# Kernel optimization log

Hardware: AMD Instinct MI355X
Metric: run time of the kernel (lower is better)

Reference implementation:

```python
import jax, jax.numpy as jnp
import numpy as np

B, T, D_IN, H = 1024, 512, 32, 64


def setup_inputs() -> dict:
    key = jax.random.key(0)
    ks = jax.random.split(key, 16)
    s_in = 1.0 / np.sqrt(H)  # torch LSTM init scale 1/sqrt(hidden)
    inp = {
        "x": jax.random.normal(ks[0], (B, T, D_IN), dtype=jnp.float32),
        # layer 0
        "Wih0": jax.random.uniform(ks[1], (4 * H, D_IN), minval=-s_in, maxval=s_in),
        "Whh0": jax.random.uniform(ks[2], (4 * H, H), minval=-s_in, maxval=s_in),
        "bih0": jax.random.uniform(ks[3], (4 * H,), minval=-s_in, maxval=s_in),
        "bhh0": jax.random.uniform(ks[4], (4 * H,), minval=-s_in, maxval=s_in),
        # layer 1
        "Wih1": jax.random.uniform(ks[5], (4 * H, H), minval=-s_in, maxval=s_in),
        "Whh1": jax.random.uniform(ks[6], (4 * H, H), minval=-s_in, maxval=s_in),
        "bih1": jax.random.uniform(ks[7], (4 * H,), minval=-s_in, maxval=s_in),
        "bhh1": jax.random.uniform(ks[8], (4 * H,), minval=-s_in, maxval=s_in),
        # head: Linear(H, H//2) -> ReLU -> Linear(H//2, 1)
        "W1": jax.random.uniform(ks[9], (H // 2, H), minval=-s_in, maxval=s_in),
        "b1": jax.random.uniform(ks[10], (H // 2,), minval=-s_in, maxval=s_in),
        "W2": jax.random.uniform(ks[11], (1, H // 2), minval=-1.0 / np.sqrt(H // 2), maxval=1.0 / np.sqrt(H // 2)),
        "b2": jax.random.uniform(ks[12], (1,), minval=-1.0 / np.sqrt(H // 2), maxval=1.0 / np.sqrt(H // 2)),
    }
    return inp


def _lstm_layer(x, Wih, Whh, bih, bhh):
    # x: [B, T, D]; returns all hidden states [B, T, H]
    b = x.shape[0]
    xT = jnp.swapaxes(x, 0, 1)  # [T, B, D]
    h0 = jnp.zeros((b, H), dtype=x.dtype)
    c0 = jnp.zeros((b, H), dtype=x.dtype)
    bias = bih + bhh

    def step(carry, xt):
        h, c = carry
        z = xt @ Wih.T + h @ Whh.T + bias  # [B, 4H]
        i, f, g, o = jnp.split(z, 4, axis=-1)  # torch gate order: i, f, g, o
        i = jax.nn.sigmoid(i)
        f = jax.nn.sigmoid(f)
        g = jnp.tanh(g)
        o = jax.nn.sigmoid(o)
        c = f * c + i * g
        h = o * jnp.tanh(c)
        return (h, c), h

    _, hs = jax.lax.scan(step, (h0, c0), xT)
    return jnp.swapaxes(hs, 0, 1)  # [B, T, H]


def reference(x, Wih0, Whh0, bih0, bhh0, Wih1, Whh1, bih1, bhh1, W1, b1, W2, b2):
    h1 = _lstm_layer(x, Wih0, Whh0, bih0, bhh0)   # [B, T, H]
    h2 = _lstm_layer(h1, Wih1, Whh1, bih1, bhh1)  # [B, T, H] (dropout = identity, eval)
    last = h2[:, -1]                              # [B, H]
    hidden = jax.nn.relu(last @ W1.T + b1)        # [B, H//2]
    out = hidden @ W2.T + b2                      # [B, 1]
    return out[:, 0]                              # [B]
```

## Files before the change

kernel.cpp:

```cpp
#include <hip/hip_runtime.h>

#define T       512
#define DIN     32
#define HCELLS  64
#define NB      16
#define TB      512
#define GRID    64

typedef _Float16 half8  __attribute__((ext_vector_type(8)));
typedef _Float16 half4v __attribute__((ext_vector_type(4)));
typedef _Float16 half2v __attribute__((ext_vector_type(2)));
typedef float    float4v __attribute__((ext_vector_type(4)));

#define STRX    40
#define STRH    72
#define XH_OFF  0
#define H0H_OFF (2*16*STRX)
#define H1H_OFF (H0H_OFF + 2*16*STRH)
#define SB_HALFS (H1H_OFF + 2*16*STRH)

#define LOG2E   1.44269504f
#define SLOG2E  2.88539008f

__device__ __forceinline__ int xidx(int p, int n, int k) { return (p * 16 + n) * STRX + k; }
__device__ __forceinline__ int hidx(int p, int n, int k) { return (p * 16 + n) * STRH + k; }

__device__ __forceinline__ void cvt8(const float* v, half8& hi) {
    #pragma unroll
    for (int e = 0; e < 8; ++e) hi[e] = (_Float16)v[e];
}

__device__ __forceinline__ void cell_update(const float4v acc[4], float* cs,
                                            half4v& hh, float* hout)
{
    #pragma unroll
    for (int r = 0; r < 4; ++r) {
        float ei = __builtin_amdgcn_exp2f(acc[0][r]);
        float ef = __builtin_amdgcn_exp2f(acc[1][r]);
        float G2 = __builtin_amdgcn_exp2f(acc[2][r]);
        float I  = 1.0f + ei, F = 1.0f + ef;
        float Gp = 1.0f + G2;
        float Gms = fmaf(SLOG2E, G2, -SLOG2E);
        float P   = I * Gp;
        float num = fmaf(F, Gms, cs[r] * P);
        float csn = num * __builtin_amdgcn_rcpf(F * P);
        csn = fminf(fmaxf(csn, -50.0f), 50.0f);
        cs[r] = csn;
        float eo = __builtin_amdgcn_exp2f(acc[3][r]);
        float C2 = __builtin_amdgcn_exp2f(csn);
        float O  = 1.0f + eo;
        float Cp = 1.0f + C2, Cm = C2 - 1.0f;
        float h  = Cm * __builtin_amdgcn_rcpf(O * Cp);
        if (hout) hout[r] = h;
        hh[r] = (_Float16)h;
    }
}

__global__ void __launch_bounds__(TB, 2)
lstm2_mfma_kernel(const float* __restrict__ x,
                  const float* __restrict__ Wih0, const float* __restrict__ Whh0,
                  const float* __restrict__ bih0, const float* __restrict__ bhh0,
                  const float* __restrict__ Wih1, const float* __restrict__ Whh1,
                  const float* __restrict__ bih1, const float* __restrict__ bhh1,
                  const float* __restrict__ W1,   const float* __restrict__ b1,
                  const float* __restrict__ W2,   const float* __restrict__ b2,
                  float* __restrict__ out)
{
    const int tid  = threadIdx.x;
    const int wid  = tid >> 6;
    const int grp  = wid >> 2;
    const int wl   = wid & 3;
    const int lane = tid & 63;
    const int n16  = lane & 15;
    const int q    = lane >> 4;
    const int j0   = wl * 16 + q * 4;
    const int b0   = blockIdx.x * NB;

    __shared__ __align__(16) _Float16 SB[SB_HALFS];
    __shared__ __align__(16) float HS[16 * 68 + 16 * 33];

    const float gsc[4] = {-LOG2E, -LOG2E, SLOG2E, -LOG2E};

    half8 ah[4][4];
    float4v biasv[4];

    #pragma unroll
    for (int l = 0; l < 4; ++l) {
        const int row = (l * 4 + wl) * 16 + n16;
        const float g = gsc[l];
        float v[8];
        if (grp == 0) {
            {
                const float4* p = (const float4*)(Wih0 + row * DIN + q * 8);
                float4 u0 = p[0], u1 = p[1];
                v[0]=g*u0.x; v[1]=g*u0.y; v[2]=g*u0.z; v[3]=g*u0.w;
                v[4]=g*u1.x; v[5]=g*u1.y; v[6]=g*u1.z; v[7]=g*u1.w;
                cvt8(v, ah[l][0]);
            }
            #pragma unroll
            for (int kt = 1; kt < 3; ++kt) {
                const float4* p = (const float4*)(Whh0 + row * HCELLS + (kt - 1) * 32 + q * 8);
                float4 u0 = p[0], u1 = p[1];
                v[0]=g*u0.x; v[1]=g*u0.y; v[2]=g*u0.z; v[3]=g*u0.w;
                v[4]=g*u1.x; v[5]=g*u1.y; v[6]=g*u1.z; v[7]=g*u1.w;
                cvt8(v, ah[l][kt]);
            }
            const int r0 = l * 64 + j0;
            float4v bi = *(const float4v*)(bih0 + r0);
            float4v bh = *(const float4v*)(bhh0 + r0);
            biasv[l] = (bi + bh) * g;
        } else {
            #pragma unroll
            for (int kt = 0; kt < 4; ++kt) {
                const float* base = (kt < 2) ? (Wih1 + row * HCELLS + kt * 32)
                                             : (Whh1 + row * HCELLS + (kt - 2) * 32);
                const float4* p = (const float4*)(base + q * 8);
                float4 u0 = p[0], u1 = p[1];
                v[0]=g*u0.x; v[1]=g*u0.y; v[2]=g*u0.z; v[3]=g*u0.w;
                v[4]=g*u1.x; v[5]=g*u1.y; v[6]=g*u1.z; v[7]=g*u1.w;
                cvt8(v, ah[l][kt]);
            }
            const int r0 = l * 64 + j0;
            float4v bi = *(const float4v*)(bih1 + r0);
            float4v bh = *(const float4v*)(bhh1 + r0);
            biasv[l] = (bi + bh) * g;
        }
    }

    for (int i = tid; i < SB_HALFS / 2; i += TB) ((int*)SB)[i] = 0;

    const int nx = tid >> 4;
    const int kp = (tid & 15) * 2;
    const float* xp0 = (grp == 0) ? (x + (size_t)(b0 + nx) * T * DIN + kp) : nullptr;
    __syncthreads();
    if (grp == 0) {
        float2 xv = *(const float2*)xp0;
        half2v hi = {(_Float16)xv.x, (_Float16)xv.y};
        *(half2v*)&SB[XH_OFF + xidx(0, nx, kp)] = hi;
    }
    __syncthreads();

    float cs[4] = {0, 0, 0, 0};
    float hlast[4];
    const float* xp = (grp == 0) ? (xp0 + DIN) : nullptr;

    #pragma unroll 2
    for (int t = 0; t < T; ++t) {
        const int pr = t & 1, pw = pr ^ 1;

        if (grp == 0) {
            float2 xv;
            const bool havex = (t + 1 < T);
            if (havex) xv = *(const float2*)xp;
            xp += DIN;

            float4v acc[4];
            #pragma unroll
            for (int l = 0; l < 4; ++l) acc[l] = biasv[l];
            {
                half8 bh = *(const half8*)&SB[XH_OFF + xidx(pr, n16, q * 8)];
                #pragma unroll
                for (int l = 0; l < 4; ++l)
                    acc[l] = __builtin_amdgcn_mfma_f32_16x16x32_f16(ah[l][0], bh, acc[l], 0, 0, 0);
            }
            #pragma unroll
            for (int kt = 1; kt < 3; ++kt) {
                half8 bh = *(const half8*)&SB[H0H_OFF + hidx(pr, n16, (kt - 1) * 32 + q * 8)];
                #pragma unroll
                for (int l = 0; l < 4; ++l)
                    acc[l] = __builtin_amdgcn_mfma_f32_16x16x32_f16(ah[l][kt], bh, acc[l], 0, 0, 0);
            }
            half4v hh;
            cell_update(acc, cs, hh, nullptr);
            *(half4v*)&SB[H0H_OFF + hidx(pw, n16, j0)] = hh;
            if (havex) {
                half2v hi = {(_Float16)xv.x, (_Float16)xv.y};
                *(half2v*)&SB[XH_OFF + xidx(pw, nx, kp)] = hi;
            }
        } else if (t > 0) {
            float4v acc[4];
            #pragma unroll
            for (int l = 0; l < 4; ++l) acc[l] = biasv[l];
            #pragma unroll
            for (int kt = 0; kt < 4; ++kt) {
                half8 bh = (kt < 2)
                    ? *(const half8*)&SB[H0H_OFF + hidx(pr, n16, kt * 32 + q * 8)]
                    : *(const half8*)&SB[H1H_OFF + hidx(pw, n16, (kt - 2) * 32 + q * 8)];
                #pragma unroll
                for (int l = 0; l < 4; ++l)
                    acc[l] = __builtin_amdgcn_mfma_f32_16x16x32_f16(ah[l][kt], bh, acc[l], 0, 0, 0);
            }
            half4v hh;
            cell_update(acc, cs, hh, nullptr);
            *(half4v*)&SB[H1H_OFF + hidx(pr, n16, j0)] = hh;
        }
        __syncthreads();
    }

    float* h1f = HS;
    float* hid = HS + 16 * 68;
    if (grp == 1) {
        float4v acc[4];
        #pragma unroll
        for (int l = 0; l < 4; ++l) acc[l] = biasv[l];
        #pragma unroll
        for (int kt = 0; kt < 4; ++kt) {
            half8 bh = (kt < 2)
                ? *(const half8*)&SB[H0H_OFF + hidx(0, n16, kt * 32 + q * 8)]
                : *(const half8*)&SB[H1H_OFF + hidx(1, n16, (kt - 2) * 32 + q * 8)];
            #pragma unroll
            for (int l = 0; l < 4; ++l)
                acc[l] = __builtin_amdgcn_mfma_f32_16x16x32_f16(ah[l][kt], bh, acc[l], 0, 0, 0);
        }
        half4v hh;
        cell_update(acc, cs, hh, hlast);
        *(float4*)&h1f[n16 * 68 + j0] = *(const float4*)hlast;
    }
    __syncthreads();

    if (tid < 256) {
        const int n2 = tid >> 4, m = tid & 15;
        float s0 = b1[m], s1 = b1[m + 16];
        const float* w0p = W1 + m * HCELLS;
        const float* w1p = W1 + (m + 16) * HCELLS;
        #pragma unroll
        for (int j = 0; j < HCELLS; ++j) {
            float hv = h1f[n2 * 68 + j];
            s0 = fmaf(w0p[j], hv, s0);
            s1 = fmaf(w1p[j], hv, s1);
        }
        hid[n2 * 33 + m]      = fmaxf(s0, 0.0f);
        hid[n2 * 33 + m + 16] = fmaxf(s1, 0.0f);
    }
    __syncthreads();

    if (tid < NB) {
        float s = b2[0];
        #pragma unroll
        for (int m = 0; m < 32; ++m) s = fmaf(W2[m], hid[tid * 33 + m], s);
        out[b0 + tid] = s;
    }
}

extern "C" void kernel_launch(void* const* d_in, const int* in_sizes, int n_in,
                              void* d_out, int out_size, void* d_ws, size_t ws_size,
                              hipStream_t stream) {
    const float* x    = (const float*)d_in[0];
    const float* Wih0 = (const float*)d_in[1];
    const float* Whh0 = (const float*)d_in[2];
    const float* bih0 = (const float*)d_in[3];
    const float* bhh0 = (const float*)d_in[4];
    const float* Wih1 = (const float*)d_in[5];
    const float* Whh1 = (const float*)d_in[6];
    const float* bih1 = (const float*)d_in[7];
    const float* bhh1 = (const float*)d_in[8];
    const float* W1   = (const float*)d_in[9];
    const float* b1   = (const float*)d_in[10];
    const float* W2   = (const float*)d_in[11];
    const float* b2   = (const float*)d_in[12];
    float* out = (float*)d_out;

    hipLaunchKernelGGL(lstm2_mfma_kernel, dim3(GRID), dim3(TB), 0, stream,
                       x, Wih0, Whh0, bih0, bhh0, Wih1, Whh1, bih1, bhh1,
                       W1, b1, W2, b2, out);
}
```

Before: 447.5 us.

## Duplicate MFMA waves so each wave runs half the LSTM cell update

Doubles the block to 1024 threads. Each of the 4 gate-tile waves per layer now has a twin that recomputes the same MFMAs but applies the elementwise cell update to only 2 of its 4 accumulator rows. This halves the serial transcendental work per wave on the recurrent critical path, at the cost of duplicated MFMA work, more waves and registers per block, and a larger barrier on every timestep. The launch-bounds occupancy hint is raised to 4 to match.

```diff
diff --git a/kernel.cpp b/kernel.cpp
--- a/kernel.cpp
+++ b/kernel.cpp
@@ -4,11 +4,10 @@
 #define DIN     32
 #define HCELLS  64
 #define NB      16
-#define TB      512
+#define TB      1024
 #define GRID    64
 
 typedef _Float16 half8  __attribute__((ext_vector_type(8)));
-typedef _Float16 half4v __attribute__((ext_vector_type(4)));
 typedef _Float16 half2v __attribute__((ext_vector_type(2)));
 typedef float    float4v __attribute__((ext_vector_type(4)));
 
@@ -30,11 +29,12 @@
     for (int e = 0; e < 8; ++e) hi[e] = (_Float16)v[e];
 }
 
-__device__ __forceinline__ void cell_update(const float4v acc[4], float* cs,
-                                            half4v& hh, float* hout)
+__device__ __forceinline__ void cell_update2(const float4v acc[4], int r0, float* cs,
+                                             half2v& hh, float* hout)
 {
     #pragma unroll
-    for (int r = 0; r < 4; ++r) {
+    for (int e = 0; e < 2; ++e) {
+        const int r = r0 + e;
         float ei = __builtin_amdgcn_exp2f(acc[0][r]);
         float ef = __builtin_amdgcn_exp2f(acc[1][r]);
         float G2 = __builtin_amdgcn_exp2f(acc[2][r]);
@@ -42,21 +42,21 @@
         float Gp = 1.0f + G2;
         float Gms = fmaf(SLOG2E, G2, -SLOG2E);
         float P   = I * Gp;
-        float num = fmaf(F, Gms, cs[r] * P);
+        float num = fmaf(F, Gms, cs[e] * P);
         float csn = num * __builtin_amdgcn_rcpf(F * P);
         csn = fminf(fmaxf(csn, -50.0f), 50.0f);
-        cs[r] = csn;
+        cs[e] = csn;
         float eo = __builtin_amdgcn_exp2f(acc[3][r]);
         float C2 = __builtin_amdgcn_exp2f(csn);
         float O  = 1.0f + eo;
         float Cp = 1.0f + C2, Cm = C2 - 1.0f;
         float h  = Cm * __builtin_amdgcn_rcpf(O * Cp);
-        if (hout) hout[r] = h;
-        hh[r] = (_Float16)h;
-    }
-}
-
-__global__ void __launch_bounds__(TB, 2)
+        if (hout) hout[e] = h;
+        hh[e] = (_Float16)h;
+    }
+}
+
+__global__ void __launch_bounds__(TB, 4)
 lstm2_mfma_kernel(const float* __restrict__ x,
                   const float* __restrict__ Wih0, const float* __restrict__ Whh0,
                   const float* __restrict__ bih0, const float* __restrict__ bhh0,
@@ -68,12 +68,14 @@
 {
     const int tid  = threadIdx.x;
     const int wid  = tid >> 6;
-    const int grp  = wid >> 2;
+    const int grp  = wid >> 3;
     const int wl   = wid & 3;
+    const int dup  = (wid >> 2) & 1;
     const int lane = tid & 63;
     const int n16  = lane & 15;
     const int q    = lane >> 4;
     const int j0   = wl * 16 + q * 4;
+    const int jr   = j0 + 2 * dup;
     const int b0   = blockIdx.x * NB;
 
     __shared__ __align__(16) _Float16 SB[SB_HALFS];
@@ -129,20 +131,21 @@
 
     for (int i = tid; i < SB_HALFS / 2; i += TB) ((int*)SB)[i] = 0;
 
-    const int nx = tid >> 4;
+    const bool isldr = (tid < 256);
+    const int nx = (tid >> 4) & 15;
     const int kp = (tid & 15) * 2;
-    const float* xp0 = (grp == 0) ? (x + (size_t)(b0 + nx) * T * DIN + kp) : nullptr;
-    __syncthreads();
-    if (grp == 0) {
+    const float* xp0 = isldr ? (x + (size_t)(b0 + nx) * T * DIN + kp) : nullptr;
+    __syncthreads();
+    if (isldr) {
         float2 xv = *(const float2*)xp0;
         half2v hi = {(_Float16)xv.x, (_Float16)xv.y};
         *(half2v*)&SB[XH_OFF + xidx(0, nx, kp)] = hi;
     }
     __syncthreads();
 
-    float cs[4] = {0, 0, 0, 0};
-    float hlast[4];
-    const float* xp = (grp == 0) ? (xp0 + DIN) : nullptr;
+    float cs[2] = {0, 0};
+    float hlast[2];
+    const float* xp = isldr ? (xp0 + DIN) : nullptr;
 
     #pragma unroll 2
     for (int t = 0; t < T; ++t) {
@@ -150,9 +153,9 @@
 
         if (grp == 0) {
             float2 xv;
-            const bool havex = (t + 1 < T);
+            const bool havex = isldr && (t + 1 < T);
             if (havex) xv = *(const float2*)xp;
-            xp += DIN;
+            if (isldr) xp += DIN;
 
             float4v acc[4];
             #pragma unroll
@@ -170,9 +173,9 @@
                 for (int l = 0; l < 4; ++l)
                     acc[l] = __builtin_amdgcn_mfma_f32_16x16x32_f16(ah[l][kt], bh, acc[l], 0, 0, 0);
             }
-            half4v hh;
-            cell_update(acc, cs, hh, nullptr);
-            *(half4v*)&SB[H0H_OFF + hidx(pw, n16, j0)] = hh;
+            half2v hh;
+            cell_update2(acc, 2 * dup, cs, hh, nullptr);
+            *(half2v*)&SB[H0H_OFF + hidx(pw, n16, jr)] = hh;
             if (havex) {
                 half2v hi = {(_Float16)xv.x, (_Float16)xv.y};
                 *(half2v*)&SB[XH_OFF + xidx(pw, nx, kp)] = hi;
@@ -190,9 +193,9 @@
                 for (int l = 0; l < 4; ++l)
                     acc[l] = __builtin_amdgcn_mfma_f32_16x16x32_f16(ah[l][kt], bh, acc[l], 0, 0, 0);
             }
-            half4v hh;
-            cell_update(acc, cs, hh, nullptr);
-            *(half4v*)&SB[H1H_OFF + hidx(pr, n16, j0)] = hh;
+            half2v hh;
+            cell_update2(acc, 2 * dup, cs, hh, nullptr);
+            *(half2v*)&SB[H1H_OFF + hidx(pr, n16, jr)] = hh;
         }
         __syncthreads();
     }
@@ -212,9 +215,9 @@
             for (int l = 0; l < 4; ++l)
                 acc[l] = __builtin_amdgcn_mfma_f32_16x16x32_f16(ah[l][kt], bh, acc[l], 0, 0, 0);
         }
-        half4v hh;
-        cell_update(acc, cs, hh, hlast);
-        *(float4*)&h1f[n16 * 68 + j0] = *(const float4*)hlast;
+        half2v hh;
+        cell_update2(acc, 2 * dup, cs, hh, hlast);
+        *(float2*)&h1f[n16 * 68 + jr] = *(const float2*)hlast;
     }
     __syncthreads();
 
```

New measurement: 946.6 us. +111.5%, slower.
